# Performance work log

Measured on AMD Instinct MI355X. Metric: run time of the kernel, lower is better.

The kernel has to match this reference:

```python
import jax, jax.numpy as jnp
import numpy as np

N = 50000   # nodes per node type
D = 256     # in_dim == out_dim
H = 8       # num heads
DK = D // H # 32
E = 500000  # edges per edge type
LN_EPS = 1e-5


def setup_inputs() -> dict:
    key = jax.random.key(0)
    ks = jax.random.split(key, 16)
    w = lambda k, shape: jax.random.normal(k, shape, dtype=jnp.float32) * 0.05
    xav = np.sqrt(6.0 / (DK + DK))
    return {
        'feats': jax.random.normal(ks[0], (2, N, D), dtype=jnp.float32),
        'Wk': w(ks[1], (2, D, D)), 'bk': jnp.zeros((2, D), jnp.float32),
        'Wq': w(ks[2], (2, D, D)), 'bq': jnp.zeros((2, D), jnp.float32),
        'Wv': w(ks[3], (2, D, D)), 'bv': jnp.zeros((2, D), jnp.float32),
        'Wa': w(ks[4], (2, D, D)), 'ba': jnp.zeros((2, D), jnp.float32),
        'ln_w': jnp.ones((2, D), jnp.float32), 'ln_b': jnp.zeros((2, D), jnp.float32),
        'skip': jnp.ones((2,), jnp.float32),
        'mu': jnp.ones((2, H), jnp.float32),
        'w_att': jax.random.uniform(ks[5], (2, H, DK, DK), jnp.float32, -xav, xav),
        'w_msg': jax.random.uniform(ks[6], (2, H, DK, DK), jnp.float32, -xav, xav),
        'src': jax.random.randint(ks[7], (2, E), 0, N, dtype=jnp.int32),
        'dst': jax.random.randint(ks[8], (2, E), 0, N, dtype=jnp.int32),
    }


def _edge_softmax(scores, seg, n):
    # scores: (E, H); softmax over edges sharing the same destination node
    m = jax.ops.segment_max(scores, seg, num_segments=n)          # (N, H)
    e = jnp.exp(scores - m[seg])
    s = jax.ops.segment_sum(e, seg, num_segments=n)               # (N, H)
    return e / s[seg]


def _forward(feats, Wk, bk, Wq, bq, Wv, bv, Wa, ba, ln_w, ln_b, skip,
             mu, w_att, w_msg, src, dst):
    # canonical etypes: 0 = author->paper, 1 = paper->author
    stypes, dtypes = (0, 1), (1, 0)
    scale = 1.0 / jnp.sqrt(jnp.asarray(DK, feats.dtype))
    h = [None, None]
    for et in range(2):
        st, dt = stypes[et], dtypes[et]
        s_idx, d_idx = src[et], dst[et]
        k = (feats[st] @ Wk[st] + bk[st]).reshape(N, H, DK)
        k = jnp.einsum('nhi,hij->nhj', k, w_att[et])
        v = (feats[st] @ Wv[st] + bv[st]).reshape(N, H, DK)
        v = jnp.einsum('nhi,hij->nhj', v, w_msg[et])
        q = (feats[dt] @ Wq[dt] + bq[dt]).reshape(N, H, DK)
        t = jnp.einsum('ehd,ehd->eh', q[d_idx], k[s_idx])         # (E, H)
        attn = _edge_softmax(t * mu[et] * scale, d_idx, N)        # (E, H)
        msg = v[s_idx] * attn[..., None]                          # (E, H, DK)
        h[dt] = jax.ops.segment_sum(msg, d_idx, num_segments=N).reshape(N, D)
    h = jnp.stack(h)  # (2, N, D); each ntype receives from exactly one etype

    trans = jnp.einsum('tnd,tde->tne', h, Wa) + ba[:, None, :]
    alpha = jax.nn.sigmoid(skip)[:, None, None]
    out = alpha * trans + (1.0 - alpha) * feats
    mean = out.mean(-1, keepdims=True)
    var = out.var(-1, keepdims=True)
    out = (out - mean) * jax.lax.rsqrt(var + LN_EPS)
    return out * ln_w[:, None, :] + ln_b[:, None, :]


def reference(feats, Wk, bk, Wq, bq, Wv, bv, Wa, ba, ln_w, ln_b, skip,
              mu, w_att, w_msg, src, dst):
    return _forward(feats, Wk, bk, Wq, bq, Wv, bv, Wa, ba, ln_w, ln_b, skip,
                    mu, w_att, w_msg, src, dst)
```

## Files before the change

kernel.cpp:

```cpp
#include <hip/hip_runtime.h>
#include <hip/hip_bf16.h>

#define D 256
#define H 8
#define DK 32

typedef unsigned short ushort_t;
typedef unsigned int uint_t;
typedef __attribute__((ext_vector_type(4))) float floatx4;
typedef __attribute__((ext_vector_type(8))) short shortx8;
typedef __attribute__((ext_vector_type(8))) unsigned short ushortx8;

typedef __attribute__((address_space(3))) void lds_void_t;
typedef const __attribute__((address_space(1))) void gbl_void_t;

__device__ __forceinline__ float b2f(ushort_t u) {
    return __uint_as_float(((uint_t)u) << 16);
}
__device__ __forceinline__ ushort_t f2b(float f) {
    uint_t u = __float_as_uint(f);
    uint_t r = (u + 0x7FFFu + ((u >> 16) & 1u)) >> 16;
    return (ushort_t)r;
}
__device__ __forceinline__ void async_cp16(const void* g, void* l) {
    __builtin_amdgcn_global_load_lds((gbl_void_t*)g, (lds_void_t*)l, 16, 0, 0);
}

__global__ void cvt_bf16(const float* __restrict__ in, ushort_t* __restrict__ out, size_t n4) {
    size_t i = (size_t)blockIdx.x * blockDim.x + threadIdx.x;
    if (i >= n4) return;
    float4 v = ((const float4*)in)[i];
    ushort4 o;
    o.x = f2b(v.x); o.y = f2b(v.y); o.z = f2b(v.z); o.w = f2b(v.w);
    ((ushort4*)out)[i] = o;
}

__global__ void zero_int(int* __restrict__ p, int n) {
    int i = blockIdx.x * blockDim.x + threadIdx.x;
    if (i < n) p[i] = 0;
}

__global__ void fold_weights(const float* __restrict__ Wk, const float* __restrict__ bk,
                             const float* __restrict__ Wv, const float* __restrict__ bv,
                             const float* __restrict__ w_att, const float* __restrict__ w_msg,
                             float* __restrict__ Wkc, float* __restrict__ bkc,
                             float* __restrict__ Wvc, float* __restrict__ bvc) {
    int r = blockIdx.x, et = blockIdx.y, which = blockIdx.z;
    int tid = threadIdx.x;
    const float* Wsrc = (which ? Wv : Wk) + (size_t)et * D * D + (size_t)r * D;
    const float* wt   = (which ? w_msg : w_att) + (size_t)et * H * DK * DK;
    float* Wdst = (which ? Wvc : Wkc) + (size_t)et * D * D;
    __shared__ float wrow[D];
    wrow[tid] = Wsrc[tid];
    __syncthreads();
    int h = tid >> 5, j = tid & 31;
    const float* wth = wt + h * DK * DK;
    float acc = 0.f;
#pragma unroll 8
    for (int i = 0; i < DK; i++) acc += wrow[h * 32 + i] * wth[i * 32 + j];
    Wdst[(size_t)r * D + tid] = acc;
    if (r == 0) {
        const float* bsrc = (which ? bv : bk) + et * D;
        float* bdst = (which ? bvc : bkc) + et * D;
        float bacc = 0.f;
#pragma unroll 8
        for (int i = 0; i < DK; i++) bacc += bsrc[h * 32 + i] * wth[i * 32 + j];
        bdst[tid] = bacc;
    }
}

__global__ void pack_weights(const float* __restrict__ Wq, const float* __restrict__ bq,
                             const float* __restrict__ Wkc, const float* __restrict__ bkc,
                             const float* __restrict__ Wvc, const float* __restrict__ bvc,
                             const float* __restrict__ Wa,
                             ushort_t* __restrict__ WT_all, ushort_t* __restrict__ WaT,
                             float* __restrict__ bias_all) {
    int idx = blockIdx.x * blockDim.x + threadIdx.x;
    const int NW = 2 * 768 * 256;
    if (idx < NW) {
        int t = idx / (768 * 256);
        int rem = idx - t * 768 * 256;
        int n = rem >> 8, k = rem & 255;
        int sec = n >> 8, nn = n & 255;
        const float* W = (sec == 0) ? Wq : (sec == 1) ? Wkc : Wvc;
        WT_all[idx] = f2b(W[(size_t)t * D * D + (size_t)k * D + nn]);
    } else if (idx < NW + 2 * 256 * 256) {
        int r = idx - NW;
        int t = r / (256 * 256);
        int rem = r - t * 256 * 256;
        int n = rem >> 8, k = rem & 255;
        WaT[r] = f2b(Wa[(size_t)t * D * D + (size_t)k * D + n]);
    }
    if (idx < 2 * 768) {
        int t = idx / 768, n = idx % 768;
        int sec = n >> 8, nn = n & 255;
        const float* b = (sec == 0) ? bq : (sec == 1) ? bkc : bvc;
        bias_all[idx] = b[t * D + nn];
    }
}

#define TM 128
#define TN 128
#define TKK 32
__launch_bounds__(256)
__global__ void gemm_mfma(const ushort_t* __restrict__ A, int lda,
                          const ushort_t* __restrict__ BT,
                          const float* __restrict__ bias,
                          ushort_t* __restrict__ C, int ldc, int M) {
    __shared__ ushort_t As[TM * TKK];
    __shared__ ushort_t Bs[TN * TKK];
    int tid = threadIdx.x;
    int w = tid >> 6, lane = tid & 63;
    int bm = blockIdx.x * TM;
    int bn = blockIdx.y * TN;
    int wm = (w & 1) * 64, wn = (w >> 1) * 64;

    floatx4 acc[4][4] = {};

    int srow = lane >> 2;
    int scol = (lane & 3) * 8;

    for (int kc = 0; kc < 256; kc += TKK) {
#pragma unroll
        for (int j = 0; j < 2; j++) {
            int r = w * 32 + j * 16;
            int gr = bm + r + srow; if (gr >= M) gr = M - 1;
            async_cp16(A + (size_t)gr * lda + kc + scol, As + r * TKK);
            int gn = bn + r + srow;
            async_cp16(BT + (size_t)gn * 256 + kc + scol, Bs + r * TKK);
        }
        __builtin_amdgcn_s_waitcnt(0x0F70);
        __syncthreads();

        int fr = lane & 15, fq = lane >> 4;
        shortx8 af[4], bf[4];
#pragma unroll
        for (int i = 0; i < 4; i++)
            af[i] = *(const shortx8*)(As + (wm + i * 16 + fr) * TKK + fq * 8);
#pragma unroll
        for (int j = 0; j < 4; j++)
            bf[j] = *(const shortx8*)(Bs + (wn + j * 16 + fr) * TKK + fq * 8);
#pragma unroll
        for (int i = 0; i < 4; i++)
#pragma unroll
            for (int j = 0; j < 4; j++)
                acc[i][j] = __builtin_amdgcn_mfma_f32_16x16x32_bf16(af[i], bf[j], acc[i][j], 0, 0, 0);
        __syncthreads();
    }

    int fr = lane & 15, fq = lane >> 4;
#pragma unroll
    for (int i = 0; i < 4; i++) {
#pragma unroll
        for (int j = 0; j < 4; j++) {
            int col = bn + wn + j * 16 + fr;
            float bv = bias[col];
#pragma unroll
            for (int r = 0; r < 4; r++) {
                int row = bm + wm + i * 16 + fq * 4 + r;
                if (row < M) C[(size_t)row * ldc + col] = f2b(acc[i][j][r] + bv);
            }
        }
    }
}

__global__ void count_deg(const int* __restrict__ dst, int* __restrict__ deg,
                          int N, int E) {
    int i = blockIdx.x * blockDim.x + threadIdx.x;
    if (i >= 2 * E) return;
    int et = i / E, e = i - et * E;
    int d = dst[(size_t)et * E + e];
    atomicAdd(&deg[(1 - et) * N + d], 1);
}

__launch_bounds__(1024)
__global__ void scan_deg(const int* __restrict__ deg, int* __restrict__ row_ptr,
                         int* __restrict__ cursor, int n) {
    __shared__ int warp_scan[16];
    __shared__ int running;
    int tid = threadIdx.x;
    int lane = tid & 63, w = tid >> 6;
    if (tid == 0) running = 0;
    __syncthreads();
    for (int base = 0; base < n; base += 1024) {
        int i = base + tid;
        int v = (i < n) ? deg[i] : 0;
        int run = running;
        int x = v;
#pragma unroll
        for (int off = 1; off < 64; off <<= 1) {
            int y = __shfl_up(x, off);
            if (lane >= off) x += y;
        }
        if (lane == 63) warp_scan[w] = x;
        __syncthreads();
        if (tid < 16) {
            int t = warp_scan[tid];
#pragma unroll
            for (int off = 1; off < 16; off <<= 1) {
                int y = __shfl_up(t, off);
                if (tid >= off) t += y;
            }
            warp_scan[tid] = t;
        }
        __syncthreads();
        int woff = w ? warp_scan[w - 1] : 0;
        if (i < n) {
            int excl = run + woff + x - v;
            row_ptr[i] = excl;
            cursor[i] = excl;
        }
        int total = warp_scan[15];
        __syncthreads();
        if (tid == 0) running = run + total;
        __syncthreads();
    }
    if (tid == 0) row_ptr[n] = running;
}

__global__ void fill_edges(const int* __restrict__ src, const int* __restrict__ dst,
                           int* __restrict__ cursor, int* __restrict__ ebuf,
                           int N, int E) {
    int i = blockIdx.x * blockDim.x + threadIdx.x;
    if (i >= 2 * E) return;
    int et = i / E, e = i - et * E;
    int d = dst[(size_t)et * E + e];
    int s = src[(size_t)et * E + e];
    int pos = atomicAdd(&cursor[(1 - et) * N + d], 1);
    ebuf[pos] = s;
}

__launch_bounds__(256)
__global__ void node_aggregate(ushort_t* __restrict__ QKV, const float* __restrict__ mu,
                               const int* __restrict__ row_ptr, const int* __restrict__ ebuf,
                               int N) {
    int wid = (blockIdx.x * blockDim.x + threadIdx.x) >> 6;
    int lane = threadIdx.x & 63;
    if (wid >= 2 * N) return;
    int dt = (wid >= N) ? 1 : 0;
    int et = 1 - dt;
    int l = lane & 31;
    int half = lane >> 5;
    int h = l >> 2;

    ushortx8 qu = ((const ushortx8*)(QKV + (size_t)wid * 768))[l];
    float q0 = b2f(qu[0]), q1 = b2f(qu[1]), q2 = b2f(qu[2]), q3 = b2f(qu[3]);
    float q4 = b2f(qu[4]), q5 = b2f(qu[5]), q6 = b2f(qu[6]), q7 = b2f(qu[7]);
    float sc = mu[et * H + h] * 0.17677669529663687f;
    int beg = row_ptr[wid], end = row_ptr[wid + 1];
    const ushort_t* KVb = QKV + (size_t)et * N * 768;

    float a0 = 0.f, a1 = 0.f, a2 = 0.f, a3 = 0.f;
    float a4 = 0.f, a5 = 0.f, a6 = 0.f, a7 = 0.f, ssum = 0.f;

    int idx = beg + half;
    ushortx8 ku0 = {}, vu0 = {};
    int s1v = 0;
    if (idx < end) {
        int s0v = ebuf[idx];
        int i2 = idx + 2;
        s1v = ebuf[i2 < end ? i2 : idx];
        const ushort_t* srow = KVb + (size_t)s0v * 768 + l * 8;
        ku0 = *(const ushortx8*)(srow + 256);
        vu0 = *(const ushortx8*)(srow + 512);
    }
    while (idx < end) {
        int i2 = idx + 2;
        ushortx8 ku1 = ku0, vu1 = vu0;
        int s2v = s1v;
        if (i2 < end) {
            int i4 = idx + 4;
            s2v = ebuf[i4 < end ? i4 : i2];
            const ushort_t* srow = KVb + (size_t)s1v * 768 + l * 8;
            ku1 = *(const ushortx8*)(srow + 256);
            vu1 = *(const ushortx8*)(srow + 512);
        }
        float p = q0 * b2f(ku0[0]) + q1 * b2f(ku0[1]) + q2 * b2f(ku0[2]) + q3 * b2f(ku0[3])
                + q4 * b2f(ku0[4]) + q5 * b2f(ku0[5]) + q6 * b2f(ku0[6]) + q7 * b2f(ku0[7]);
        p += __shfl_xor(p, 1);
        p += __shfl_xor(p, 2);
        float ex = __expf(p * sc);
        ssum += ex;
        a0 += ex * b2f(vu0[0]); a1 += ex * b2f(vu0[1]);
        a2 += ex * b2f(vu0[2]); a3 += ex * b2f(vu0[3]);
        a4 += ex * b2f(vu0[4]); a5 += ex * b2f(vu0[5]);
        a6 += ex * b2f(vu0[6]); a7 += ex * b2f(vu0[7]);
        ku0 = ku1; vu0 = vu1; s1v = s2v;
        idx = i2;
    }
    ssum += __shfl_xor(ssum, 32);
    a0 += __shfl_xor(a0, 32); a1 += __shfl_xor(a1, 32);
    a2 += __shfl_xor(a2, 32); a3 += __shfl_xor(a3, 32);
    a4 += __shfl_xor(a4, 32); a5 += __shfl_xor(a5, 32);
    a6 += __shfl_xor(a6, 32); a7 += __shfl_xor(a7, 32);
    float r = (ssum > 0.f) ? 1.0f / ssum : 0.0f;
    if (half == 0) {
        ushortx8 hv;
        hv[0] = f2b(a0 * r); hv[1] = f2b(a1 * r);
        hv[2] = f2b(a2 * r); hv[3] = f2b(a3 * r);
        hv[4] = f2b(a4 * r); hv[5] = f2b(a5 * r);
        hv[6] = f2b(a6 * r); hv[7] = f2b(a7 * r);
        ((ushortx8*)(QKV + (size_t)wid * 768))[l] = hv;
    }
}

__launch_bounds__(256)
__global__ void skip_ln(const ushort_t* __restrict__ trans, const float* __restrict__ feats,
                        const float* __restrict__ lnw, const float* __restrict__ lnb,
                        const float* __restrict__ skip, float* __restrict__ out, int N) {
    int wid = (blockIdx.x * blockDim.x + threadIdx.x) >> 6;
    int lane = threadIdx.x & 63;
    if (wid >= 2 * N) return;
    int t = (wid >= N) ? 1 : 0;
    float alpha = 1.0f / (1.0f + __expf(-skip[t]));
    float beta = 1.0f - alpha;
    size_t base = (size_t)wid * D;
    ushort4 tu = ((const ushort4*)(trans + base))[lane];
    float4 fu = ((const float4*)(feats + base))[lane];
    float x0 = alpha * b2f(tu.x) + beta * fu.x;
    float x1 = alpha * b2f(tu.y) + beta * fu.y;
    float x2 = alpha * b2f(tu.z) + beta * fu.z;
    float x3 = alpha * b2f(tu.w) + beta * fu.w;
    float s  = x0 + x1 + x2 + x3;
    float sq = x0 * x0 + x1 * x1 + x2 * x2 + x3 * x3;
#pragma unroll
    for (int off = 1; off < 64; off <<= 1) {
        s  += __shfl_xor(s,  off);
        sq += __shfl_xor(sq, off);
    }
    float mean = s * (1.0f / 256.0f);
    float var  = sq * (1.0f / 256.0f) - mean * mean;
    float r = rsqrtf(var + 1e-5f);
    float4 w4 = ((const float4*)(lnw + t * D))[lane];
    float4 b4 = ((const float4*)(lnb + t * D))[lane];
    float4 o;
    o.x = (x0 - mean) * r * w4.x + b4.x;
    o.y = (x1 - mean) * r * w4.y + b4.y;
    o.z = (x2 - mean) * r * w4.z + b4.z;
    o.w = (x3 - mean) * r * w4.w + b4.w;
    ((float4*)(out + base))[lane] = o;
}

extern "C" void kernel_launch(void* const* d_in, const int* in_sizes, int n_in,
                              void* d_out, int out_size, void* d_ws, size_t ws_size,
                              hipStream_t stream) {
    const float* feats = (const float*)d_in[0];
    const float* Wk    = (const float*)d_in[1];
    const float* bk    = (const float*)d_in[2];
    const float* Wq    = (const float*)d_in[3];
    const float* bq    = (const float*)d_in[4];
    const float* Wv    = (const float*)d_in[5];
    const float* bv    = (const float*)d_in[6];
    const float* Wa    = (const float*)d_in[7];
    const float* ba    = (const float*)d_in[8];
    const float* ln_w  = (const float*)d_in[9];
    const float* ln_b  = (const float*)d_in[10];
    const float* skip  = (const float*)d_in[11];
    const float* mu    = (const float*)d_in[12];
    const float* w_att = (const float*)d_in[13];
    const float* w_msg = (const float*)d_in[14];
    const int*   src   = (const int*)d_in[15];
    const int*   dst   = (const int*)d_in[16];
    float* out = (float*)d_out;

    const int N = in_sizes[0] / (2 * D);
    const int E = in_sizes[15] / 2;
    const int NN = 2 * N;
    const size_t ND2 = 2 * (size_t)N * D;

    float* ws = (float*)d_ws;
    size_t off = 0;
    float* Wkc  = ws + off; off += 2 * (size_t)D * D;
    float* Wvc  = ws + off; off += 2 * (size_t)D * D;
    float* bkc  = ws + off; off += 2 * D;
    float* bvc  = ws + off; off += 2 * D;
    float* bias_all = ws + off; off += 2 * 768;
    ushort_t* WT_all = (ushort_t*)(ws + off); off += 2 * 768 * 256 / 2;
    ushort_t* WaT    = (ushort_t*)(ws + off); off += 2 * 256 * 256 / 2;
    ushort_t* featsb = (ushort_t*)(ws + off); off += ND2 / 2;
    ushort_t* QKV    = (ushort_t*)(ws + off); off += 2 * (size_t)N * 768 / 2;
    int* deg     = (int*)(ws + off); off += NN;
    int* row_ptr = (int*)(ws + off); off += NN + 1;
    int* cursor  = (int*)(ws + off); off += NN + 1;
    int* ebuf    = (int*)(ws + off); off += 2 * (size_t)E;

    zero_int<<<(NN + 255) / 256, 256, 0, stream>>>(deg, NN);
    count_deg<<<(2 * E + 255) / 256, 256, 0, stream>>>(dst, deg, N, E);
    scan_deg<<<1, 1024, 0, stream>>>(deg, row_ptr, cursor, NN);
    fill_edges<<<(2 * E + 255) / 256, 256, 0, stream>>>(src, dst, cursor, ebuf, N, E);

    fold_weights<<<dim3(D, 2, 2), 256, 0, stream>>>(Wk, bk, Wv, bv, w_att, w_msg,
                                                    Wkc, bkc, Wvc, bvc);
    pack_weights<<<(2 * 768 * 256 + 2 * 256 * 256 + 255) / 256, 256, 0, stream>>>(
        Wq, bq, Wkc, bkc, Wvc, bvc, Wa, WT_all, WaT, bias_all);

    cvt_bf16<<<(unsigned)((ND2 / 4 + 255) / 256), 256, 0, stream>>>(feats, featsb, ND2 / 4);

    dim3 qkv_grid((N + TM - 1) / TM, 768 / TN);
    for (int t = 0; t < 2; t++)
        gemm_mfma<<<qkv_grid, 256, 0, stream>>>(featsb + (size_t)t * N * D, D,
                                                WT_all + (size_t)t * 768 * 256,
                                                bias_all + t * 768,
                                                QKV + (size_t)t * N * 768, 768, N);

    node_aggregate<<<(NN * 64 + 255) / 256, 256, 0, stream>>>(QKV, mu, row_ptr, ebuf, N);

    ushort_t* transb = featsb;
    dim3 tr_grid((N + TM - 1) / TM, 256 / TN);
    for (int t = 0; t < 2; t++)
        gemm_mfma<<<tr_grid, 256, 0, stream>>>(QKV + (size_t)t * N * 768, 768,
                                               WaT + (size_t)t * 256 * 256,
                                               ba + t * 256,
                                               transb + (size_t)t * N * D, D, N);

    skip_ln<<<(NN * 64 + 255) / 256, 256, 0, stream>>>(transb, feats, ln_w, ln_b, skip, out, N);
}
```

Measured before the change: 748.1 us.

## Parallelize degree scan, remap GEMM workgroups per XCD, pack bf16 math

Replaces the single-block serial prefix scan over 100k node degrees with a three-kernel block scan (block-local scan, top-level scan of block sums, apply), so the scan no longer runs on one workgroup. Remaps GEMM workgroup IDs so that tiles scheduled on the same XCD are contiguous, aiming for better L2 reuse of A/B tiles. Rewrites the attention aggregation inner loop to unpack bf16 pairs into float2 vectors, allowing packed FMA instructions. Adds two extra kernel launches for the scan.

```diff
diff --git a/kernel.cpp b/kernel.cpp
--- a/kernel.cpp
+++ b/kernel.cpp
@@ -8,6 +8,7 @@
 typedef unsigned short ushort_t;
 typedef unsigned int uint_t;
 typedef __attribute__((ext_vector_type(4))) float floatx4;
+typedef __attribute__((ext_vector_type(2))) float floatx2;
 typedef __attribute__((ext_vector_type(8))) short shortx8;
 typedef __attribute__((ext_vector_type(8))) unsigned short ushortx8;
 
@@ -16,6 +17,12 @@
 
 __device__ __forceinline__ float b2f(ushort_t u) {
     return __uint_as_float(((uint_t)u) << 16);
+}
+__device__ __forceinline__ floatx2 b2x2(uint_t u) {
+    floatx2 r;
+    r.x = __uint_as_float(u << 16);
+    r.y = __uint_as_float(u & 0xffff0000u);
+    return r;
 }
 __device__ __forceinline__ ushort_t f2b(float f) {
     uint_t u = __float_as_uint(f);
@@ -111,8 +118,18 @@
     __shared__ ushort_t Bs[TN * TKK];
     int tid = threadIdx.x;
     int w = tid >> 6, lane = tid & 63;
-    int bm = blockIdx.x * TM;
-    int bn = blockIdx.y * TN;
+
+    int nwg  = gridDim.x * gridDim.y;
+    int orig = blockIdx.y * gridDim.x + blockIdx.x;
+    int q = nwg >> 3, r = nwg & 7;
+    int xcd = orig & 7, loc = orig >> 3;
+    int wgid = (xcd < r ? xcd * (q + 1) : r * (q + 1) + (xcd - r) * q) + loc;
+    int ncol = gridDim.y;
+    int rowt = wgid / ncol;
+    int colt = wgid - rowt * ncol;
+    int bm = rowt * TM;
+    int bn = colt * TN;
+
     int wm = (w & 1) * 64, wn = (w >> 1) * 64;
 
     floatx4 acc[4][4] = {};
@@ -123,11 +140,11 @@
     for (int kc = 0; kc < 256; kc += TKK) {
 #pragma unroll
         for (int j = 0; j < 2; j++) {
-            int r = w * 32 + j * 16;
-            int gr = bm + r + srow; if (gr >= M) gr = M - 1;
-            async_cp16(A + (size_t)gr * lda + kc + scol, As + r * TKK);
-            int gn = bn + r + srow;
-            async_cp16(BT + (size_t)gn * 256 + kc + scol, Bs + r * TKK);
+            int rr = w * 32 + j * 16;
+            int gr = bm + rr + srow; if (gr >= M) gr = M - 1;
+            async_cp16(A + (size_t)gr * lda + kc + scol, As + rr * TKK);
+            int gn = bn + rr + srow;
+            async_cp16(BT + (size_t)gn * 256 + kc + scol, Bs + rr * TKK);
         }
         __builtin_amdgcn_s_waitcnt(0x0F70);
         __syncthreads();
@@ -156,9 +173,9 @@
             int col = bn + wn + j * 16 + fr;
             float bv = bias[col];
 #pragma unroll
-            for (int r = 0; r < 4; r++) {
-                int row = bm + wm + i * 16 + fq * 4 + r;
-                if (row < M) C[(size_t)row * ldc + col] = f2b(acc[i][j][r] + bv);
+            for (int rr = 0; rr < 4; rr++) {
+                int row = bm + wm + i * 16 + fq * 4 + rr;
+                if (row < M) C[(size_t)row * ldc + col] = f2b(acc[i][j][rr] + bv);
             }
         }
     }
@@ -173,49 +190,58 @@
     atomicAdd(&deg[(1 - et) * N + d], 1);
 }
 
-__launch_bounds__(1024)
-__global__ void scan_deg(const int* __restrict__ deg, int* __restrict__ row_ptr,
-                         int* __restrict__ cursor, int n) {
-    __shared__ int warp_scan[16];
-    __shared__ int running;
-    int tid = threadIdx.x;
-    int lane = tid & 63, w = tid >> 6;
-    if (tid == 0) running = 0;
+__launch_bounds__(256)
+__global__ void scan_blocks(int* __restrict__ deg, int* __restrict__ bsum, int n) {
+    __shared__ int wsum[4];
+    int tid = threadIdx.x, lane = tid & 63, w = tid >> 6;
+    int i = blockIdx.x * 256 + tid;
+    int v = (i < n) ? deg[i] : 0;
+    int x = v;
+#pragma unroll
+    for (int off = 1; off < 64; off <<= 1) {
+        int y = __shfl_up(x, off);
+        if (lane >= off) x += y;
+    }
+    if (lane == 63) wsum[w] = x;
     __syncthreads();
-    for (int base = 0; base < n; base += 1024) {
-        int i = base + tid;
-        int v = (i < n) ? deg[i] : 0;
-        int run = running;
-        int x = v;
-#pragma unroll
-        for (int off = 1; off < 64; off <<= 1) {
-            int y = __shfl_up(x, off);
-            if (lane >= off) x += y;
-        }
-        if (lane == 63) warp_scan[w] = x;
-        __syncthreads();
-        if (tid < 16) {
-            int t = warp_scan[tid];
-#pragma unroll
-            for (int off = 1; off < 16; off <<= 1) {
-                int y = __shfl_up(t, off);
-                if (tid >= off) t += y;
-            }
-            warp_scan[tid] = t;
-        }
-        __syncthreads();
-        int woff = w ? warp_scan[w - 1] : 0;
-        if (i < n) {
-            int excl = run + woff + x - v;
-            row_ptr[i] = excl;
-            cursor[i] = excl;
-        }
-        int total = warp_scan[15];
-        __syncthreads();
-        if (tid == 0) running = run + total;
-        __syncthreads();
-    }
-    if (tid == 0) row_ptr[n] = running;
+    int add = 0;
+    if (w > 0) add += wsum[0];
+    if (w > 1) add += wsum[1];
+    if (w > 2) add += wsum[2];
+    int incl = x + add;
+    if (i < n) deg[i] = incl - v;
+    if (tid == 255) bsum[blockIdx.x] = incl;
+}
+
+__launch_bounds__(512)
+__global__ void scan_tops(int* __restrict__ bsum, int* __restrict__ row_ptr,
+                          int nb, int n) {
+    __shared__ int wsum[8];
+    int tid = threadIdx.x, lane = tid & 63, w = tid >> 6;
+    int v = (tid < nb) ? bsum[tid] : 0;
+    int x = v;
+#pragma unroll
+    for (int off = 1; off < 64; off <<= 1) {
+        int y = __shfl_up(x, off);
+        if (lane >= off) x += y;
+    }
+    if (lane == 63) wsum[w] = x;
+    __syncthreads();
+    int add = 0;
+    for (int j = 0; j < w; j++) add += wsum[j];
+    int incl = x + add;
+    if (tid < nb) bsum[tid] = incl - v;
+    if (tid == nb - 1) row_ptr[n] = incl;
+}
+
+__launch_bounds__(256)
+__global__ void scan_apply(const int* __restrict__ excl, const int* __restrict__ bsum,
+                           int* __restrict__ row_ptr, int* __restrict__ cursor, int n) {
+    int i = blockIdx.x * 256 + threadIdx.x;
+    if (i >= n) return;
+    int e = excl[i] + bsum[blockIdx.x];
+    row_ptr[i] = e;
+    cursor[i] = e;
 }
 
 __global__ void fill_edges(const int* __restrict__ src, const int* __restrict__ dst,
@@ -243,63 +269,66 @@
     int half = lane >> 5;
     int h = l >> 2;
 
-    ushortx8 qu = ((const ushortx8*)(QKV + (size_t)wid * 768))[l];
-    float q0 = b2f(qu[0]), q1 = b2f(qu[1]), q2 = b2f(qu[2]), q3 = b2f(qu[3]);
-    float q4 = b2f(qu[4]), q5 = b2f(qu[5]), q6 = b2f(qu[6]), q7 = b2f(qu[7]);
+    uint4 qu = ((const uint4*)(QKV + (size_t)wid * 768))[l];
+    floatx2 q01 = b2x2(qu.x), q23 = b2x2(qu.y), q45 = b2x2(qu.z), q67 = b2x2(qu.w);
     float sc = mu[et * H + h] * 0.17677669529663687f;
     int beg = row_ptr[wid], end = row_ptr[wid + 1];
     const ushort_t* KVb = QKV + (size_t)et * N * 768;
 
-    float a0 = 0.f, a1 = 0.f, a2 = 0.f, a3 = 0.f;
-    float a4 = 0.f, a5 = 0.f, a6 = 0.f, a7 = 0.f, ssum = 0.f;
+    floatx2 a01 = {0.f, 0.f}, a23 = {0.f, 0.f}, a45 = {0.f, 0.f}, a67 = {0.f, 0.f};
+    float ssum = 0.f;
 
     int idx = beg + half;
-    ushortx8 ku0 = {}, vu0 = {};
+    uint4 ku0 = {}, vu0 = {};
     int s1v = 0;
     if (idx < end) {
         int s0v = ebuf[idx];
         int i2 = idx + 2;
         s1v = ebuf[i2 < end ? i2 : idx];
         const ushort_t* srow = KVb + (size_t)s0v * 768 + l * 8;
-        ku0 = *(const ushortx8*)(srow + 256);
-        vu0 = *(const ushortx8*)(srow + 512);
+        ku0 = *(const uint4*)(srow + 256);
+        vu0 = *(const uint4*)(srow + 512);
     }
     while (idx < end) {
         int i2 = idx + 2;
-        ushortx8 ku1 = ku0, vu1 = vu0;
+        uint4 ku1 = ku0, vu1 = vu0;
         int s2v = s1v;
         if (i2 < end) {
             int i4 = idx + 4;
             s2v = ebuf[i4 < end ? i4 : i2];
             const ushort_t* srow = KVb + (size_t)s1v * 768 + l * 8;
-            ku1 = *(const ushortx8*)(srow + 256);
-            vu1 = *(const ushortx8*)(srow + 512);
+            ku1 = *(const uint4*)(srow + 256);
+            vu1 = *(const uint4*)(srow + 512);
         }
-        float p = q0 * b2f(ku0[0]) + q1 * b2f(ku0[1]) + q2 * b2f(ku0[2]) + q3 * b2f(ku0[3])
-                + q4 * b2f(ku0[4]) + q5 * b2f(ku0[5]) + q6 * b2f(ku0[6]) + q7 * b2f(ku0[7]);
+        floatx2 pv = q01 * b2x2(ku0.x);
+        pv += q23 * b2x2(ku0.y);
+        pv += q45 * b2x2(ku0.z);
+        pv += q67 * b2x2(ku0.w);
+        float p = pv.x + pv.y;
         p += __shfl_xor(p, 1);
         p += __shfl_xor(p, 2);
         float ex = __expf(p * sc);
         ssum += ex;
-        a0 += ex * b2f(vu0[0]); a1 += ex * b2f(vu0[1]);
-        a2 += ex * b2f(vu0[2]); a3 += ex * b2f(vu0[3]);
-        a4 += ex * b2f(vu0[4]); a5 += ex * b2f(vu0[5]);
-        a6 += ex * b2f(vu0[6]); a7 += ex * b2f(vu0[7]);
+        floatx2 ex2 = {ex, ex};
+        a01 += ex2 * b2x2(vu0.x);
+        a23 += ex2 * b2x2(vu0.y);
+        a45 += ex2 * b2x2(vu0.z);
+        a67 += ex2 * b2x2(vu0.w);
         ku0 = ku1; vu0 = vu1; s1v = s2v;
         idx = i2;
     }
     ssum += __shfl_xor(ssum, 32);
-    a0 += __shfl_xor(a0, 32); a1 += __shfl_xor(a1, 32);
-    a2 += __shfl_xor(a2, 32); a3 += __shfl_xor(a3, 32);
-    a4 += __shfl_xor(a4, 32); a5 += __shfl_xor(a5, 32);
-    a6 += __shfl_xor(a6, 32); a7 += __shfl_xor(a7, 32);
+    a01.x += __shfl_xor(a01.x, 32); a01.y += __shfl_xor(a01.y, 32);
+    a23.x += __shfl_xor(a23.x, 32); a23.y += __shfl_xor(a23.y, 32);
+    a45.x += __shfl_xor(a45.x, 32); a45.y += __shfl_xor(a45.y, 32);
+    a67.x += __shfl_xor(a67.x, 32); a67.y += __shfl_xor(a67.y, 32);
     float r = (ssum > 0.f) ? 1.0f / ssum : 0.0f;
     if (half == 0) {
         ushortx8 hv;
-        hv[0] = f2b(a0 * r); hv[1] = f2b(a1 * r);
-        hv[2] = f2b(a2 * r); hv[3] = f2b(a3 * r);
-        hv[4] = f2b(a4 * r); hv[5] = f2b(a5 * r);
-        hv[6] = f2b(a6 * r); hv[7] = f2b(a7 * r);
+        hv[0] = f2b(a01.x * r); hv[1] = f2b(a01.y * r);
+        hv[2] = f2b(a23.x * r); hv[3] = f2b(a23.y * r);
+        hv[4] = f2b(a45.x * r); hv[5] = f2b(a45.y * r);
+        hv[6] = f2b(a67.x * r); hv[7] = f2b(a67.y * r);
         ((ushortx8*)(QKV + (size_t)wid * 768))[l] = hv;
     }
 }
@@ -383,10 +412,15 @@
     int* row_ptr = (int*)(ws + off); off += NN + 1;
     int* cursor  = (int*)(ws + off); off += NN + 1;
     int* ebuf    = (int*)(ws + off); off += 2 * (size_t)E;
+    int* bsum    = (int*)(ws + off); off += 512;
+
+    const int nb = (NN + 255) / 256;
 
     zero_int<<<(NN + 255) / 256, 256, 0, stream>>>(deg, NN);
     count_deg<<<(2 * E + 255) / 256, 256, 0, stream>>>(dst, deg, N, E);
-    scan_deg<<<1, 1024, 0, stream>>>(deg, row_ptr, cursor, NN);
+    scan_blocks<<<nb, 256, 0, stream>>>(deg, bsum, NN);
+    scan_tops<<<1, 512, 0, stream>>>(bsum, row_ptr, nb, NN);
+    scan_apply<<<nb, 256, 0, stream>>>(deg, bsum, row_ptr, cursor, NN);
     fill_edges<<<(2 * E + 255) / 256, 256, 0, stream>>>(src, dst, cursor, ebuf, N, E);
 
     fold_weights<<<dim3(D, 2, 2), 256, 0, stream>>>(Wk, bk, Wv, bv, w_att, w_msg,
```

Result: faster. 633.3 us (-15.3%).
